# Optimization experiments

Hardware: AMD Instinct MI355X
Metric: run time of the kernel (lower is better)

## Reference

```python
import jax, jax.numpy as jnp
import numpy as np

CONNECTIVITY_WEIGHT = 1.0
HOLE_WEIGHT = 0.5
SUBSAMPLE = 128  # original strides sequences longer than 128
N_TRIPLETS = 32


def _pairwise_dist(x):
    # x: [B, Tc, D] -> Euclidean distance matrix [B, Tc, Tc] (torch.cdist p=2)
    sqn = jnp.sum(x * x, axis=-1)  # [B, Tc]
    sq = sqn[:, :, None] + sqn[:, None, :] - 2.0 * jnp.einsum('bid,bjd->bij', x, x)
    sq = jnp.maximum(sq, 0.0)
    # safe sqrt: zero gradient at zero distance (matches torch.cdist behavior)
    sq_safe = jnp.where(sq > 0, sq, 1.0)
    return jnp.where(sq > 0, jnp.sqrt(sq_safe), 0.0)


def setup_inputs() -> dict:
    key = jax.random.key(0)
    k1, k2 = jax.random.split(key)
    B, T, D = 128, 2048, 512
    latent_batch = jax.random.normal(k1, (B, T, D), dtype=jnp.float32)
    connection_threshold = jnp.ones((1,), dtype=jnp.float32)
    triplet_idx = jax.random.randint(k2, (B, N_TRIPLETS, 3), 0, SUBSAMPLE, dtype=jnp.int32)
    return {
        'latent_batch': latent_batch,
        'connection_threshold': connection_threshold,
        'triplet_idx': triplet_idx,
    }


def reference(latent_batch, connection_threshold, triplet_idx):
    B, T, D = latent_batch.shape
    stride = max(T // SUBSAMPLE, 1)
    x = latent_batch[:, ::stride, :]  # [B, Tc, D], static slice
    Tc = x.shape[1]

    d = _pairwise_dist(x)  # [B, Tc, Tc]

    threshold = jnp.abs(connection_threshold[0]) + 0.1
    # sigmoid(-(d - thr)) == sigmoid(thr - d)
    p = jax.nn.sigmoid(threshold - d)
    conn_sum = jnp.sum(p, axis=(1, 2)) - jnp.trace(p, axis1=1, axis2=2)  # [B]
    denom = Tc * (Tc - 1) + 1e-8
    connectivity_loss = 1.0 - conn_sum / denom  # [B]

    # random-triplet hole loss
    b_idx = jnp.arange(B)[:, None]
    i0, i1, i2 = triplet_idx[..., 0], triplet_idx[..., 1], triplet_idx[..., 2]
    d01 = d[b_idx, i0, i1]  # [B, N_TRIPLETS]
    d02 = d[b_idx, i0, i2]
    d12 = d[b_idx, i1, i2]
    edges = jnp.stack([d01, d02, d12], axis=-1)  # [B, N_TRIPLETS, 3]
    edge_var = jnp.var(edges, axis=-1, ddof=1)  # torch.var default unbiased
    hole_loss = jnp.mean(jnp.exp(-edge_var), axis=-1)  # [B]

    avg_loss = (CONNECTIVITY_WEIGHT * jnp.mean(connectivity_loss)
                + HOLE_WEIGHT * jnp.mean(hole_loss))
    return avg_loss
```

## Files before the change

kernel.cpp:

```cpp
#include <hip/hip_runtime.h>
#include <math.h>

#define NB 128
#define TC 128
#define DD 512
#define TSTR 16
#define KT 64
#define NT (DD/KT)
#define XP 72
#define DST 132
#define NTRIP 32

typedef __attribute__((ext_vector_type(8))) short bf16x8;
typedef __attribute__((ext_vector_type(8))) unsigned short u16x8;
typedef __attribute__((ext_vector_type(4))) float f32x4;

__device__ __forceinline__ unsigned short f2bf(float f) {
  unsigned int u = __float_as_uint(f);
  return (unsigned short)((u + 0x7fffu + ((u >> 16) & 1u)) >> 16);
}

__device__ __forceinline__ u16x8 cvt8(float4 a, float4 b) {
  u16x8 w;
  w[0]=f2bf(a.x); w[1]=f2bf(a.y); w[2]=f2bf(a.z); w[3]=f2bf(a.w);
  w[4]=f2bf(b.x); w[5]=f2bf(b.y); w[6]=f2bf(b.z); w[7]=f2bf(b.w);
  return w;
}

__global__ __launch_bounds__(1024) void topo_fused(
    const float* __restrict__ latent,
    const float* __restrict__ thr,
    const int*   __restrict__ trip,
    float* __restrict__ partial)
{
  const int b    = blockIdx.x;
  const int tid  = threadIdx.x;
  const int lane = tid & 63;
  const int wid  = tid >> 6;
  const int wrow = (wid >> 2) * 32;
  const int wcol = (wid & 3) * 32;

  __shared__ __align__(16) unsigned short xt[2][TC][XP];
  __shared__ float dmat[TC][DST];
  __shared__ float sqn[TC];
  __shared__ float wred[16];

  const float* xb = latent + (size_t)b * (2048 * 512);

  const int srow = tid >> 3;
  const int skc  = (tid & 7) * 8;
  const float* sp = xb + (size_t)srow * (TSTR * DD) + skc;

  float4 pA[4][2], pB[4][2];
#pragma unroll
  for (int t = 0; t < 4; ++t) {
    pA[t][0] = *reinterpret_cast<const float4*>(sp + t * KT);
    pA[t][1] = *reinterpret_cast<const float4*>(sp + t * KT + 4);
  }
#pragma unroll
  for (int t = 0; t < 4; ++t) {
    pB[t][0] = *reinterpret_cast<const float4*>(sp + (t + 4) * KT);
    pB[t][1] = *reinterpret_cast<const float4*>(sp + (t + 4) * KT + 4);
  }

  u16x8 rb[8];
#pragma unroll
  for (int t = 0; t < 4; ++t) rb[t] = cvt8(pA[t][0], pA[t][1]);

  f32x4 acc[2][2];
#pragma unroll
  for (int i = 0; i < 2; ++i)
#pragma unroll
    for (int j = 0; j < 2; ++j)
#pragma unroll
      for (int r = 0; r < 4; ++r) acc[i][j][r] = 0.f;

  const int r0  = wrow + (lane & 15);
  const int c0  = wcol + (lane & 15);
  const int kk0 = (lane >> 4) << 3;

  *reinterpret_cast<u16x8*>(&xt[0][srow][skc]) = rb[0];
  __syncthreads();

  for (int t = 0; t < NT; ++t) {
    if (t == 3) {
#pragma unroll
      for (int q = 0; q < 4; ++q) rb[4 + q] = cvt8(pB[q][0], pB[q][1]);
    }
    if (t + 1 < NT)
      *reinterpret_cast<u16x8*>(&xt[(t + 1) & 1][srow][skc]) = rb[t + 1];
    const int cur = t & 1;
#pragma unroll
    for (int sub = 0; sub < 2; ++sub) {
      const int kk = sub * 32 + kk0;
      bf16x8 a0 = *reinterpret_cast<const bf16x8*>(&xt[cur][r0][kk]);
      bf16x8 a1 = *reinterpret_cast<const bf16x8*>(&xt[cur][r0 + 16][kk]);
      bf16x8 b0 = *reinterpret_cast<const bf16x8*>(&xt[cur][c0][kk]);
      bf16x8 b1 = *reinterpret_cast<const bf16x8*>(&xt[cur][c0 + 16][kk]);
      acc[0][0] = __builtin_amdgcn_mfma_f32_16x16x32_bf16(a0, b0, acc[0][0], 0, 0, 0);
      acc[0][1] = __builtin_amdgcn_mfma_f32_16x16x32_bf16(a0, b1, acc[0][1], 0, 0, 0);
      acc[1][0] = __builtin_amdgcn_mfma_f32_16x16x32_bf16(a1, b0, acc[1][0], 0, 0, 0);
      acc[1][1] = __builtin_amdgcn_mfma_f32_16x16x32_bf16(a1, b1, acc[1][1], 0, 0, 0);
    }
    __syncthreads();
  }

  const int rbase = (lane >> 4) << 2;
  const int cidx  = lane & 15;
#pragma unroll
  for (int fr = 0; fr < 2; ++fr)
#pragma unroll
    for (int fc = 0; fc < 2; ++fc)
#pragma unroll
      for (int reg = 0; reg < 4; ++reg) {
        int grow = wrow + fr * 16 + rbase + reg;
        int gcol = wcol + fc * 16 + cidx;
        if (grow == gcol) sqn[grow] = acc[fr][fc][reg];
      }
  __syncthreads();

  const float thv = fabsf(thr[0]) + 0.1f;
  float psum = 0.f;
#pragma unroll
  for (int fr = 0; fr < 2; ++fr)
#pragma unroll
    for (int fc = 0; fc < 2; ++fc)
#pragma unroll
      for (int reg = 0; reg < 4; ++reg) {
        int grow = wrow + fr * 16 + rbase + reg;
        int gcol = wcol + fc * 16 + cidx;
        float g  = acc[fr][fc][reg];
        float sq = fmaxf(sqn[grow] + sqn[gcol] - 2.f * g, 0.f);
        float d  = sqrtf(sq);
        dmat[grow][gcol] = d;
        if (grow != gcol) psum += 1.f / (1.f + __expf(d - thv));
      }

#pragma unroll
  for (int off = 32; off; off >>= 1) psum += __shfl_down(psum, off, 64);
  if (lane == 0) wred[wid] = psum;
  __syncthreads();

  if (wid == 0) {
    float h = 0.f;
    if (lane < NTRIP) {
      const int* tp = trip + ((size_t)b * NTRIP + lane) * 3;
      int i0 = tp[0], i1 = tp[1], i2 = tp[2];
      float e0 = dmat[i0][i1], e1 = dmat[i0][i2], e2 = dmat[i1][i2];
      float m  = (e0 + e1 + e2) * (1.f / 3.f);
      float d0 = e0 - m, d1 = e1 - m, d2 = e2 - m;
      float v  = (d0 * d0 + d1 * d1 + d2 * d2) * 0.5f;
      h = __expf(-v);
    }
#pragma unroll
    for (int off = 32; off; off >>= 1) h += __shfl_down(h, off, 64);
    if (lane == 0) {
      float conn = 0.f;
#pragma unroll
      for (int w = 0; w < 16; ++w) conn += wred[w];
      partial[b]      = 1.f - conn / 16256.0f;
      partial[NB + b] = h * (1.f / NTRIP);
    }
  }
}

__global__ void topo_final(const float* __restrict__ partial, float* __restrict__ out)
{
  const int t = threadIdx.x;
  float v = partial[t] + 0.5f * partial[NB + t];
#pragma unroll
  for (int off = 32; off; off >>= 1) v += __shfl_down(v, off, 64);
  __shared__ float s2[2];
  if ((t & 63) == 0) s2[t >> 6] = v;
  __syncthreads();
  if (t == 0) out[0] = (s2[0] + s2[1]) * (1.f / NB);
}

extern "C" void kernel_launch(void* const* d_in, const int* in_sizes, int n_in,
                              void* d_out, int out_size, void* d_ws, size_t ws_size,
                              hipStream_t stream) {
  const float* latent = (const float*)d_in[0];
  const float* thr    = (const float*)d_in[1];
  const int*   trip   = (const int*)d_in[2];
  float* partial = (float*)d_ws;

  topo_fused<<<NB, 1024, 0, stream>>>(latent, thr, trip, partial);
  topo_final<<<1, 128, 0, stream>>>(partial, (float*)d_out);
}
```

Baseline: 19.49 us.

## Split each batch Gram matrix into two row-half blocks across 256 workgroups

Each batch is now handled by two 512-thread blocks, each computing half the rows of the 128x128 distance matrix, so the grid grows from 128 to 256 workgroups to fill more CUs. Because a block no longer owns the diagonal, squared norms are computed in fp32 from the loaded data instead of read off the Gram diagonal. Triplet edges are written to the workspace and the hole-loss variance is finished in the final kernel. Each block still loads and converts the full 128x512 slice, so global reads double, and the fp32 norms are now combined with a bf16 Gram, which slightly changes numerics near the diagonal.

```diff
diff --git a/kernel.cpp b/kernel.cpp
--- a/kernel.cpp
+++ b/kernel.cpp
@@ -3,6 +3,7 @@
 
 #define NB 128
 #define TC 128
+#define HALF 64
 #define DD 512
 #define TSTR 16
 #define KT 64
@@ -27,13 +28,16 @@
   return w;
 }
 
-__global__ __launch_bounds__(1024) void topo_fused(
+__global__ __launch_bounds__(512, 2) void topo_half(
     const float* __restrict__ latent,
     const float* __restrict__ thr,
     const int*   __restrict__ trip,
-    float* __restrict__ partial)
+    float* __restrict__ ws_psum,
+    float* __restrict__ ws_edge)
 {
-  const int b    = blockIdx.x;
+  const int blk  = blockIdx.x;
+  const int s    = blk >> 7;
+  const int b    = blk & 127;
   const int tid  = threadIdx.x;
   const int lane = tid & 63;
   const int wid  = tid >> 6;
@@ -41,31 +45,40 @@
   const int wcol = (wid & 3) * 32;
 
   __shared__ __align__(16) unsigned short xt[2][TC][XP];
-  __shared__ float dmat[TC][DST];
+  __shared__ float dmat[HALF][DST];
   __shared__ float sqn[TC];
-  __shared__ float wred[16];
+  __shared__ float wred[8];
 
   const float* xb = latent + (size_t)b * (2048 * 512);
 
-  const int srow = tid >> 3;
-  const int skc  = (tid & 7) * 8;
+  const int srow = tid >> 2;
+  const int skc  = (tid & 3) * 16;
   const float* sp = xb + (size_t)srow * (TSTR * DD) + skc;
 
-  float4 pA[4][2], pB[4][2];
+  float4 pA[4][4], pB[4][4];
+#pragma unroll
+  for (int t = 0; t < 4; ++t)
+#pragma unroll
+    for (int q = 0; q < 4; ++q)
+      pA[t][q] = *reinterpret_cast<const float4*>(sp + t * KT + q * 4);
+#pragma unroll
+  for (int t = 0; t < 4; ++t)
+#pragma unroll
+    for (int q = 0; q < 4; ++q)
+      pB[t][q] = *reinterpret_cast<const float4*>(sp + (t + 4) * KT + q * 4);
+
+  float ssq = 0.f;
+  u16x8 rb[16];
 #pragma unroll
   for (int t = 0; t < 4; ++t) {
-    pA[t][0] = *reinterpret_cast<const float4*>(sp + t * KT);
-    pA[t][1] = *reinterpret_cast<const float4*>(sp + t * KT + 4);
-  }
-#pragma unroll
-  for (int t = 0; t < 4; ++t) {
-    pB[t][0] = *reinterpret_cast<const float4*>(sp + (t + 4) * KT);
-    pB[t][1] = *reinterpret_cast<const float4*>(sp + (t + 4) * KT + 4);
-  }
-
-  u16x8 rb[8];
-#pragma unroll
-  for (int t = 0; t < 4; ++t) rb[t] = cvt8(pA[t][0], pA[t][1]);
+    rb[2 * t]     = cvt8(pA[t][0], pA[t][1]);
+    rb[2 * t + 1] = cvt8(pA[t][2], pA[t][3]);
+#pragma unroll
+    for (int q = 0; q < 4; ++q) {
+      float4 v = pA[t][q];
+      ssq += v.x * v.x + v.y * v.y + v.z * v.z + v.w * v.w;
+    }
+  }
 
   f32x4 acc[2][2];
 #pragma unroll
@@ -75,20 +88,31 @@
 #pragma unroll
       for (int r = 0; r < 4; ++r) acc[i][j][r] = 0.f;
 
-  const int r0  = wrow + (lane & 15);
+  const int r0  = s * HALF + wrow + (lane & 15);
   const int c0  = wcol + (lane & 15);
   const int kk0 = (lane >> 4) << 3;
 
-  *reinterpret_cast<u16x8*>(&xt[0][srow][skc]) = rb[0];
+  *reinterpret_cast<u16x8*>(&xt[0][srow][skc])     = rb[0];
+  *reinterpret_cast<u16x8*>(&xt[0][srow][skc + 8]) = rb[1];
   __syncthreads();
 
   for (int t = 0; t < NT; ++t) {
     if (t == 3) {
 #pragma unroll
-      for (int q = 0; q < 4; ++q) rb[4 + q] = cvt8(pB[q][0], pB[q][1]);
-    }
-    if (t + 1 < NT)
-      *reinterpret_cast<u16x8*>(&xt[(t + 1) & 1][srow][skc]) = rb[t + 1];
+      for (int u = 0; u < 4; ++u) {
+        rb[8 + 2 * u] = cvt8(pB[u][0], pB[u][1]);
+        rb[9 + 2 * u] = cvt8(pB[u][2], pB[u][3]);
+#pragma unroll
+        for (int q = 0; q < 4; ++q) {
+          float4 v = pB[u][q];
+          ssq += v.x * v.x + v.y * v.y + v.z * v.z + v.w * v.w;
+        }
+      }
+    }
+    if (t + 1 < NT) {
+      *reinterpret_cast<u16x8*>(&xt[(t + 1) & 1][srow][skc])     = rb[2 * t + 2];
+      *reinterpret_cast<u16x8*>(&xt[(t + 1) & 1][srow][skc + 8]) = rb[2 * t + 3];
+    }
     const int cur = t & 1;
 #pragma unroll
     for (int sub = 0; sub < 2; ++sub) {
@@ -105,20 +129,13 @@
     __syncthreads();
   }
 
+  ssq += __shfl_xor(ssq, 1, 64);
+  ssq += __shfl_xor(ssq, 2, 64);
+  if ((tid & 3) == 0) sqn[srow] = ssq;
+  __syncthreads();
+
   const int rbase = (lane >> 4) << 2;
   const int cidx  = lane & 15;
-#pragma unroll
-  for (int fr = 0; fr < 2; ++fr)
-#pragma unroll
-    for (int fc = 0; fc < 2; ++fc)
-#pragma unroll
-      for (int reg = 0; reg < 4; ++reg) {
-        int grow = wrow + fr * 16 + rbase + reg;
-        int gcol = wcol + fc * 16 + cidx;
-        if (grow == gcol) sqn[grow] = acc[fr][fc][reg];
-      }
-  __syncthreads();
-
   const float thv = fabsf(thr[0]) + 0.1f;
   float psum = 0.f;
 #pragma unroll
@@ -127,13 +144,17 @@
     for (int fc = 0; fc < 2; ++fc)
 #pragma unroll
       for (int reg = 0; reg < 4; ++reg) {
-        int grow = wrow + fr * 16 + rbase + reg;
-        int gcol = wcol + fc * 16 + cidx;
-        float g  = acc[fr][fc][reg];
-        float sq = fmaxf(sqn[grow] + sqn[gcol] - 2.f * g, 0.f);
-        float d  = sqrtf(sq);
-        dmat[grow][gcol] = d;
-        if (grow != gcol) psum += 1.f / (1.f + __expf(d - thv));
+        int growL = wrow + fr * 16 + rbase + reg;
+        int grow  = s * HALF + growL;
+        int gcol  = wcol + fc * 16 + cidx;
+        float d = 0.f;
+        if (grow != gcol) {
+          float g  = acc[fr][fc][reg];
+          float sq = fmaxf(sqn[grow] + sqn[gcol] - 2.f * g, 0.f);
+          d = sqrtf(sq);
+          psum += 1.f / (1.f + __expf(d - thv));
+        }
+        dmat[growL][gcol] = d;
       }
 
 #pragma unroll
@@ -142,38 +163,66 @@
   __syncthreads();
 
   if (wid == 0) {
-    float h = 0.f;
     if (lane < NTRIP) {
       const int* tp = trip + ((size_t)b * NTRIP + lane) * 3;
-      int i0 = tp[0], i1 = tp[1], i2 = tp[2];
-      float e0 = dmat[i0][i1], e1 = dmat[i0][i2], e2 = dmat[i1][i2];
-      float m  = (e0 + e1 + e2) * (1.f / 3.f);
-      float d0 = e0 - m, d1 = e1 - m, d2 = e2 - m;
-      float v  = (d0 * d0 + d1 * d1 + d2 * d2) * 0.5f;
-      h = __expf(-v);
-    }
-#pragma unroll
-    for (int off = 32; off; off >>= 1) h += __shfl_down(h, off, 64);
+      const int i0 = tp[0], i1 = tp[1], i2 = tp[2];
+      const size_t ebase = ((size_t)b * NTRIP + lane) * 3;
+      int ps[3] = {i0, i0, i1};
+      int qs[3] = {i1, i2, i2};
+#pragma unroll
+      for (int e = 0; e < 3; ++e) {
+        int p = ps[e], q = qs[e];
+        int mx = p > q ? p : q, mn = p > q ? q : p;
+        if ((mx >> 6) == s)
+          ws_edge[ebase + e] = (mx == mn) ? 0.f : dmat[mx - s * HALF][mn];
+      }
+    }
     if (lane == 0) {
       float conn = 0.f;
 #pragma unroll
-      for (int w = 0; w < 16; ++w) conn += wred[w];
-      partial[b]      = 1.f - conn / 16256.0f;
-      partial[NB + b] = h * (1.f / NTRIP);
-    }
-  }
-}
-
-__global__ void topo_final(const float* __restrict__ partial, float* __restrict__ out)
+      for (int w = 0; w < 8; ++w) conn += wred[w];
+      ws_psum[blk] = conn;
+    }
+  }
+}
+
+__global__ __launch_bounds__(1024) void topo_final(
+    const float* __restrict__ ws_psum,
+    const float* __restrict__ ws_edge,
+    float* __restrict__ out)
 {
-  const int t = threadIdx.x;
-  float v = partial[t] + 0.5f * partial[NB + t];
-#pragma unroll
-  for (int off = 32; off; off >>= 1) v += __shfl_down(v, off, 64);
-  __shared__ float s2[2];
-  if ((t & 63) == 0) s2[t >> 6] = v;
-  __syncthreads();
-  if (t == 0) out[0] = (s2[0] + s2[1]) * (1.f / NB);
+  const int t    = threadIdx.x;
+  const int lane = t & 63;
+  const int wid  = t >> 6;
+
+  float ps = (t < 2 * NB) ? ws_psum[t] : 0.f;
+  float hs = 0.f;
+#pragma unroll
+  for (int k = 0; k < 4; ++k) {
+    int id = t + 1024 * k;
+    float e0 = ws_edge[id * 3 + 0];
+    float e1 = ws_edge[id * 3 + 1];
+    float e2 = ws_edge[id * 3 + 2];
+    float m  = (e0 + e1 + e2) * (1.f / 3.f);
+    float d0 = e0 - m, d1 = e1 - m, d2 = e2 - m;
+    float v  = (d0 * d0 + d1 * d1 + d2 * d2) * 0.5f;
+    hs += __expf(-v);
+  }
+
+#pragma unroll
+  for (int off = 32; off; off >>= 1) {
+    ps += __shfl_down(ps, off, 64);
+    hs += __shfl_down(hs, off, 64);
+  }
+  __shared__ float rp[16], rh[16];
+  if (lane == 0) { rp[wid] = ps; rh[wid] = hs; }
+  __syncthreads();
+  if (t == 0) {
+    float Ps = 0.f, Hs = 0.f;
+#pragma unroll
+    for (int w = 0; w < 16; ++w) { Ps += rp[w]; Hs += rh[w]; }
+    out[0] = 1.f - Ps / (16256.f * NB) + 0.5f * (Hs / (NB * NTRIP));
+  }
 }
 
 extern "C" void kernel_launch(void* const* d_in, const int* in_sizes, int n_in,
@@ -182,8 +231,10 @@
   const float* latent = (const float*)d_in[0];
   const float* thr    = (const float*)d_in[1];
   const int*   trip   = (const int*)d_in[2];
-  float* partial = (float*)d_ws;
-
-  topo_fused<<<NB, 1024, 0, stream>>>(latent, thr, trip, partial);
-  topo_final<<<1, 128, 0, stream>>>(partial, (float*)d_out);
-}
+
+  float* ws_psum = (float*)d_ws;
+  float* ws_edge = ws_psum + 2 * NB;
+
+  topo_half<<<2 * NB, 512, 0, stream>>>(latent, thr, trip, ws_psum, ws_edge);
+  topo_final<<<1, 1024, 0, stream>>>(ws_psum, ws_edge, (float*)d_out);
+}
```

Result: faster. 18.68 us (-4.2%).
